# Kernel optimization log

Measured on AMD Instinct MI355X. Metric: run time of the kernel, lower is better.

## Reference

```python
import jax, jax.numpy as jnp
import numpy as np

NUM_CAPSULE = 10
DIM_CAPSULE = 16
ROUTINGS = 3
EPS = 1e-7  # K.epsilon()


def squash(x, axis=-1):
    sq_norm = jnp.sum(jnp.square(x), axis=axis, keepdims=True) + EPS
    coeff = jnp.sqrt(sq_norm) / (1.0 + sq_norm)
    return coeff * x


def setup_inputs() -> dict:
    key = jax.random.key(0)
    k1, k2 = jax.random.split(key)
    B, I, Din = 64, 4096, 128
    u_vecs = jax.random.normal(k1, (B, I, Din), dtype=jnp.float32)
    # glorot-ish scale for the capsule kernel (flattened conv1d kernel of size 1)
    W = jax.random.normal(k2, (Din, NUM_CAPSULE * DIM_CAPSULE), dtype=jnp.float32) * 0.06
    return {"u_vecs": u_vecs, "W": W}


def reference(u_vecs, W):
    B, I, Din = u_vecs.shape
    N, D = NUM_CAPSULE, DIM_CAPSULE
    # conv1d with kernel size 1 == per-position matmul
    u_hat = jnp.einsum('bid,dk->bik', u_vecs, W)          # [B, I, N*D]
    u_hat = u_hat.reshape(B, I, N, D).transpose(0, 2, 1, 3)  # [B, N, I, D]

    b = jnp.zeros((B, N, I), dtype=u_hat.dtype)
    outputs = None
    for i in range(ROUTINGS):
        c = jax.nn.softmax(b, axis=1)                      # softmax over num_capsule
        s = jnp.einsum('bni,bnid->bnd', c, u_hat)          # weighted sum over input caps
        outputs = squash(s)                                # [B, N, D]
        if i < ROUTINGS - 1:
            b = jnp.einsum('bnd,bnid->bni', outputs, u_hat)  # agreement logits
    return outputs
```

## Files before the change

### kernel.cpp

```cpp
#include <hip/hip_runtime.h>
#include <hip/hip_bf16.h>
#include <math.h>

#define NCAP 10
#define DCAP 16
#define DIN  128
#define NPOS 4096
#define NB   64

typedef short short8 __attribute__((ext_vector_type(8)));
typedef float floatx4 __attribute__((ext_vector_type(4)));

__device__ inline float bflo(unsigned v) { return __uint_as_float(v << 16); }
__device__ inline float bfhi(unsigned v) { return __uint_as_float(v & 0xFFFF0000u); }
__device__ inline unsigned short f2bf(float f) {
    unsigned u = __float_as_uint(f);
    return (unsigned short)((u + 0x7FFFu + ((u >> 16) & 1u)) >> 16);
}


__global__ __launch_bounds__(256) void wprep(const float* __restrict__ W,
                                             uint4* __restrict__ WTg) {
    const int cid = blockIdx.x * 256 + threadIdx.x;
    if (cid >= 2560) return;
    const int row = cid >> 4;
    const int csn = cid & 15;
    const int kc = csn ^ (row & 15);
    unsigned p[4];
    #pragma unroll
    for (int e = 0; e < 4; ++e) {
        const float a = W[(kc * 8 + e * 2) * 160 + row];
        const float b = W[(kc * 8 + e * 2 + 1) * 160 + row];
        p[e] = (unsigned)f2bf(a) | ((unsigned)f2bf(b) << 16);
    }
    WTg[cid] = make_uint4(p[0], p[1], p[2], p[3]);
}

__global__ __launch_bounds__(256) void gemm_uhat(const float* __restrict__ u,
                                                 const uint4* __restrict__ WTg,
                                                 uint2* __restrict__ uf2,
                                                 float* __restrict__ partial) {
    const int b = blockIdx.x;
    const int blk = blockIdx.y;
    const int t = threadIdx.x;
    const int l = t & 63;
    const int wv = __builtin_amdgcn_readfirstlane(t >> 6);

    __shared__ uint4 WT4[2560];

    #pragma unroll
    for (int i = 0; i < 10; ++i)
        WT4[t + i * 256] = WTg[t + i * 256];
    __syncthreads();

    float cs[4][8];
    #pragma unroll
    for (int kk = 0; kk < 4; ++kk)
        #pragma unroll
        for (int e = 0; e < 8; ++e) cs[kk][e] = 0.f;

    const short8* wt8 = (const short8*)WT4;
    const float4* u4g = (const float4*)u;

    #pragma unroll 1
    for (int mt = 0; mt < 4; ++mt) {
        const size_t row = (size_t)b * NPOS + blk * 256 + mt * 64 + wv * 16 + (l & 15);
        short8 bfr[4];
        #pragma unroll
        for (int kk = 0; kk < 4; ++kk) {
            const float4 x0 = u4g[row * 32 + kk * 8 + (l >> 4) * 2];
            const float4 x1 = u4g[row * 32 + kk * 8 + (l >> 4) * 2 + 1];
            cs[kk][0] += x0.x; cs[kk][1] += x0.y; cs[kk][2] += x0.z; cs[kk][3] += x0.w;
            cs[kk][4] += x1.x; cs[kk][5] += x1.y; cs[kk][6] += x1.z; cs[kk][7] += x1.w;
            short8 a;
            a[0] = (short)f2bf(x0.x); a[1] = (short)f2bf(x0.y);
            a[2] = (short)f2bf(x0.z); a[3] = (short)f2bf(x0.w);
            a[4] = (short)f2bf(x1.x); a[5] = (short)f2bf(x1.y);
            a[6] = (short)f2bf(x1.z); a[7] = (short)f2bf(x1.w);
            bfr[kk] = a;
        }

        const size_t cell = (((size_t)(b * 16 + blk) * 4 + mt) * 4 + wv) * 10;
        #pragma unroll 2
        for (int n = 0; n < 10; ++n) {
            floatx4 a = {0.f, 0.f, 0.f, 0.f};
            #pragma unroll
            for (int kk = 0; kk < 4; ++kk) {
                const short8 wf = wt8[(n * 16 + (l & 15)) * 16 +
                                      ((kk * 4 + (l >> 4)) ^ (l & 15))];
                a = __builtin_amdgcn_mfma_f32_16x16x32_bf16(wf, bfr[kk], a, 0, 0, 0);
            }
            uint2 pk;
            pk.x = (unsigned)f2bf(a[0]) | ((unsigned)f2bf(a[1]) << 16);
            pk.y = (unsigned)f2bf(a[2]) | ((unsigned)f2bf(a[3]) << 16);
            uf2[(cell + n) * 64 + l] = pk;
        }
    }

    __syncthreads();
    float* csbuf = (float*)WT4;
    #pragma unroll
    for (int kk = 0; kk < 4; ++kk)
        #pragma unroll
        for (int e = 0; e < 8; ++e) {
            float v = cs[kk][e];
            v += __shfl_xor(v, 1); v += __shfl_xor(v, 2);
            v += __shfl_xor(v, 4); v += __shfl_xor(v, 8);
            cs[kk][e] = v;
        }
    if ((l & 15) == 0) {
        #pragma unroll
        for (int kk = 0; kk < 4; ++kk)
            #pragma unroll
            for (int e = 0; e < 8; ++e)
                csbuf[wv * 128 + kk * 32 + (l >> 4) * 8 + e] = cs[kk][e];
    }
    __syncthreads();
    if (t < 128)
        partial[(size_t)(b * 16 + blk) * 128 + t] =
            csbuf[t] + csbuf[128 + t] + csbuf[256 + t] + csbuf[384 + t];
}

__global__ __launch_bounds__(128) void small0(const float* __restrict__ partial,
                                              const float* __restrict__ W,
                                              float* __restrict__ vbuf) {
    const int b = blockIdx.x / NCAP;
    const int n = blockIdx.x % NCAP;
    const int t = threadIdx.x;
    __shared__ float xv[DIN];
    float a = 0.f;
    #pragma unroll 4
    for (int c = 0; c < 16; ++c)
        a += partial[(size_t)(b * 16 + c) * DIN + t];
    xv[t] = a;
    __syncthreads();
    if (t < DCAP) {
        float sv = 0.f;
        for (int d = 0; d < DIN; ++d)
            sv = fmaf(xv[d], W[d * 160 + n * DCAP + t], sv);
        sv *= 0.1f;
        float nq = sv * sv;
        #pragma unroll
        for (int mm = 8; mm >= 1; mm >>= 1) nq += __shfl_xor(nq, mm, 16);
        nq += 1e-7f;
        vbuf[(size_t)(b * NCAP + n) * DCAP + t] = sv * sqrtf(nq) / (1.0f + nq);
    }
}

__global__ __launch_bounds__(256) void route_uf(const uint2* __restrict__ uf2,
                                                const float* __restrict__ vbuf,
                                                float* __restrict__ pws) {
    const int b = blockIdx.x;
    const int g = blockIdx.y;
    const int t = threadIdx.x;
    const int l = t & 63;
    const int w = __builtin_amdgcn_readfirstlane(t >> 6);

    const size_t cell = (((size_t)(b * 16 + (g >> 2)) * 4 + (g & 3)) * 4 + w) * 10;

    float vals[10][4];
    float lg[10];
    #pragma unroll
    for (int n = 0; n < 10; ++n) {
        const uint2 q = uf2[(cell + n) * 64 + l];
        vals[n][0] = bflo(q.x); vals[n][1] = bfhi(q.x);
        vals[n][2] = bflo(q.y); vals[n][3] = bfhi(q.y);
        const float4 vq = *(const float4*)&vbuf[(size_t)(b * 10 + n) * 16 + (l >> 4) * 4];
        lg[n] = vals[n][0] * vq.x + vals[n][1] * vq.y +
                vals[n][2] * vq.z + vals[n][3] * vq.w;
    }
    #pragma unroll
    for (int n = 0; n < 10; ++n) {
        lg[n] += __shfl_xor(lg[n], 16);
        lg[n] += __shfl_xor(lg[n], 32);
    }
    float m = lg[0];
    #pragma unroll
    for (int n = 1; n < 10; ++n) m = fmaxf(m, lg[n]);
    float ssum = 0.f;
    float c[10];
    #pragma unroll
    for (int n = 0; n < 10; ++n) { c[n] = __expf(lg[n] - m); ssum += c[n]; }
    const float inv = 1.0f / ssum;

    float sp[10][4];
    #pragma unroll
    for (int n = 0; n < 10; ++n) {
        const float cn = c[n] * inv;
        #pragma unroll
        for (int r = 0; r < 4; ++r) sp[n][r] = cn * vals[n][r];
    }
    #pragma unroll
    for (int n = 0; n < 10; ++n)
        #pragma unroll
        for (int r = 0; r < 4; ++r) {
            float v = sp[n][r];
            v += __shfl_xor(v, 1); v += __shfl_xor(v, 2);
            v += __shfl_xor(v, 4); v += __shfl_xor(v, 8);
            sp[n][r] = v;
        }

    __shared__ float sm[4][160];
    if ((l & 15) == 0) {
        #pragma unroll
        for (int n = 0; n < 10; ++n)
            #pragma unroll
            for (int r = 0; r < 4; ++r)
                sm[w][n * 16 + (l >> 4) * 4 + r] = sp[n][r];
    }
    __syncthreads();
    if (t < 160)
        pws[(size_t)(b * 64 + g) * 160 + t] =
            sm[0][t] + sm[1][t] + sm[2][t] + sm[3][t];
}

__global__ __launch_bounds__(256) void smallv(const float* __restrict__ pws,
                                              float* __restrict__ dst) {
    const int b = blockIdx.x;
    const int t = threadIdx.x;
    if (t >= 160) return;
    float a = 0.f;
    #pragma unroll 8
    for (int c = 0; c < 64; ++c)
        a += pws[(size_t)(b * 64 + c) * 160 + t];
    float nq = a * a;
    #pragma unroll
    for (int mm = 8; mm >= 1; mm >>= 1) nq += __shfl_xor(nq, mm, 16);
    nq += 1e-7f;
    dst[(size_t)b * 160 + t] = a * sqrtf(nq) / (1.0f + nq);
}


__global__ __launch_bounds__(256) void caps_sum(const float* __restrict__ u,
                                                float* __restrict__ partial) {
    const int b = blockIdx.x;
    const int chunk = blockIdx.y;
    const int t = threadIdx.x;
    const int v4 = t & 31;
    const int prow = t >> 5;
    const float4* up = (const float4*)u;
    const size_t posbase = (size_t)b * NPOS + chunk * 256;
    float4 acc = make_float4(0.f, 0.f, 0.f, 0.f);
    #pragma unroll 8
    for (int j = 0; j < 32; ++j) {
        float4 x = up[(posbase + prow + j * 8) * 32 + v4];
        acc.x += x.x; acc.y += x.y; acc.z += x.z; acc.w += x.w;
    }
    __shared__ float4 red[8][32];
    red[prow][v4] = acc;
    __syncthreads();
    if (t < 32) {
        float4 s = red[0][t];
        #pragma unroll
        for (int r = 1; r < 8; ++r) {
            s.x += red[r][t].x; s.y += red[r][t].y;
            s.z += red[r][t].z; s.w += red[r][t].w;
        }
        ((float4*)partial)[((size_t)b * 16 + chunk) * 32 + t] = s;
    }
}

template <int MODE>
__global__ __launch_bounds__(128) void caps_small(const float* __restrict__ src,
                                                  const float* __restrict__ W,
                                                  float* __restrict__ dst) {
    const int b = blockIdx.x / NCAP;
    const int n = blockIdx.x % NCAP;
    const int t = threadIdx.x;
    __shared__ float xv[DIN];
    __shared__ float vv[DCAP];
    float a = 0.f;
    if (MODE == 0) {
        #pragma unroll 4
        for (int c = 0; c < 16; ++c) a += src[(size_t)(b * 16 + c) * DIN + t];
    } else {
        #pragma unroll 4
        for (int c = 0; c < 16; ++c) a += src[((size_t)(b * 16 + c) * NCAP + n) * DIN + t];
    }
    xv[t] = a;
    __syncthreads();
    if (t < DCAP) {
        float sv = 0.f;
        for (int d = 0; d < DIN; ++d) sv = fmaf(xv[d], W[d * 160 + n * DCAP + t], sv);
        if (MODE == 0) sv *= 0.1f;
        float nq = sv * sv;
        #pragma unroll
        for (int mm = 8; mm >= 1; mm >>= 1) nq += __shfl_xor(nq, mm, 16);
        nq += 1e-7f;
        const float v = sv * sqrtf(nq) / (1.0f + nq);
        if (MODE == 2) dst[(size_t)(b * NCAP + n) * DCAP + t] = v;
        else vv[t] = v;
    }
    if (MODE != 2) {
        __syncthreads();
        float wd = 0.f;
        #pragma unroll
        for (int dd = 0; dd < DCAP; ++dd)
            wd = fmaf(W[t * 160 + n * DCAP + dd], vv[dd], wd);
        dst[(size_t)(b * NCAP + n) * DIN + t] = wd;
    }
}

__global__ __launch_bounds__(256, 3) void caps_route(const float* __restrict__ u,
                                                     const float* __restrict__ wsrc,
                                                     float* __restrict__ pdst) {
    const int b = blockIdx.x;
    const int tile = blockIdx.y;
    const int t = threadIdx.x;
    const int lane = t & 63;
    const int wv = __builtin_amdgcn_readfirstlane(t >> 6);
    __shared__ float4 tl4[64 * 32];
    __shared__ float lgp[4][64][11];
    float* tlf = (float*)tl4;
    const float4* wq4 = (const float4*)(wsrc + (size_t)b * (NCAP * DIN));
    float acc0[NCAP], acc1[NCAP];
    #pragma unroll
    for (int n = 0; n < NCAP; ++n) { acc0[n] = 0.f; acc1[n] = 0.f; }
    for (int s = 0; s < 4; ++s) {
        __syncthreads();
        const float4* src4 = (const float4*)u + ((size_t)b * NPOS + tile * 256 + s * 64) * 32;
        #pragma unroll
        for (int i = 0; i < 8; ++i) {
            const int q = t + i * 256;
            const int r = q >> 5, c = q & 31;
            tl4[r * 32 + (c ^ (r & 7))] = src4[q];
        }
        __syncthreads();
        float lg[NCAP];
        #pragma unroll
        for (int n = 0; n < NCAP; ++n) lg[n] = 0.f;
        #pragma unroll
        for (int j = 0; j < 8; ++j) {
            const float4 u4 = tl4[lane * 32 + wv * 8 + (j ^ (lane & 7))];
            #pragma unroll
            for (int n = 0; n < NCAP; ++n) {
                const float4 w4 = wq4[n * 32 + wv * 8 + j];
                lg[n] = fmaf(u4.x, w4.x, fmaf(u4.y, w4.y,
                        fmaf(u4.z, w4.z, fmaf(u4.w, w4.w, lg[n]))));
            }
        }
        #pragma unroll
        for (int n = 0; n < NCAP; ++n) lgp[wv][lane][n] = lg[n];
        __syncthreads();
        float c[NCAP];
        float m = -1e30f;
        #pragma unroll
        for (int n = 0; n < NCAP; ++n) {
            c[n] = lgp[0][lane][n] + lgp[1][lane][n] + lgp[2][lane][n] + lgp[3][lane][n];
            m = fmaxf(m, c[n]);
        }
        float ssum = 0.f;
        #pragma unroll
        for (int n = 0; n < NCAP; ++n) { c[n] = __expf(c[n] - m); ssum += c[n]; }
        const float inv = 1.0f / ssum;
        #pragma unroll
        for (int n = 0; n < NCAP; ++n) c[n] *= inv;
        const int col0 = lane >> 2, word = lane & 3;
        #pragma unroll
        for (int i = 0; i < 16; ++i) {
            const int p = wv * 16 + i;
            const int ca = col0 ^ (p & 7);
            const float u0 = tlf[(p * 32 + ca) * 4 + word];
            const float u1 = tlf[(p * 32 + ca + 16) * 4 + word];
            #pragma unroll
            for (int n = 0; n < NCAP; ++n) {
                const float cp = __int_as_float(
                    __builtin_amdgcn_readlane(__float_as_int(c[n]), p));
                acc0[n] = fmaf(cp, u0, acc0[n]);
                acc1[n] = fmaf(cp, u1, acc1[n]);
            }
        }
    }
    __syncthreads();
    float* red = tlf;
    #pragma unroll
    for (int n = 0; n < NCAP; ++n) {
        red[(wv * NCAP + n) * DIN + lane]      = acc0[n];
        red[(wv * NCAP + n) * DIN + lane + 64] = acc1[n];
    }
    __syncthreads();
    float* pb = pdst + (size_t)(b * 16 + tile) * (NCAP * DIN);
    for (int k = t; k < NCAP * DIN; k += 256)
        pb[k] = red[k] + red[1280 + k] + red[2560 + k] + red[3840 + k];
}

extern "C" void kernel_launch(void* const* d_in, const int* in_sizes, int n_in,
                              void* d_out, int out_size, void* d_ws, size_t ws_size,
                              hipStream_t stream) {
    const float* u = (const float*)d_in[0];
    const float* W = (const float*)d_in[1];
    float* out = (float*)d_out;
    char* wsb = (char*)d_ws;

    if (ws_size >= 86679552ull) {
        float* partial = (float*)wsb;
        float* pws     = (float*)wsb;
        float* vbuf    = (float*)(wsb + 2621440);
        uint4* WTg     = (uint4*)(wsb + 2662400);
        uint2* uf2     = (uint2*)(wsb + 2703360);

        wprep<<<10, 256, 0, stream>>>(W, WTg);
        gemm_uhat<<<dim3(NB, 16), 256, 0, stream>>>(u, WTg, uf2, partial);
        small0<<<NB * NCAP, 128, 0, stream>>>(partial, W, vbuf);
        route_uf<<<dim3(NB, 64), 256, 0, stream>>>(uf2, vbuf, pws);
        smallv<<<NB, 256, 0, stream>>>(pws, vbuf);
        route_uf<<<dim3(NB, 64), 256, 0, stream>>>(uf2, vbuf, pws);
        smallv<<<NB, 256, 0, stream>>>(pws, out);
    } else {
        float* partial = (float*)wsb;
        float* wbuf    = (float*)wsb + 131072;
        float* pws32   = (float*)wsb + 212992;
        caps_sum<<<dim3(NB, 16), 256, 0, stream>>>(u, partial);
        caps_small<0><<<NB * NCAP, 128, 0, stream>>>(partial, W, wbuf);
        caps_route<<<dim3(NB, 16), 256, 0, stream>>>(u, wbuf, pws32);
        caps_small<1><<<NB * NCAP, 128, 0, stream>>>(pws32, W, wbuf);
        caps_route<<<dim3(NB, 16), 256, 0, stream>>>(u, wbuf, pws32);
        caps_small<2><<<NB * NCAP, 128, 0, stream>>>(pws32, W, out);
    }
}
```

Measured before the change: 133.2 us.

## Drop LDS weight staging in GEMM and restructure routing via shared-memory transpose

The u_hat GEMM stops copying the full bf16 weight matrix into LDS. Each wave now reads its weight fragments straight from global memory (cache) and reuses each fragment across two row tiles, with the grid doubled to 32 blocks per batch and the partial-sum count doubled to match. The routing kernel stages the u_hat tile in LDS, computes logits per wave slice, then reduces across positions with a per-output-column loop instead of cross-lane shuffles. This removes the LDS fill and shuffle reductions but adds LDS traffic, extra barriers and a serial 64-step accumulation done by only 160 threads.

```diff
diff --git a/kernel.cpp b/kernel.cpp
--- a/kernel.cpp
+++ b/kernel.cpp
@@ -17,6 +17,7 @@
     unsigned u = __float_as_uint(f);
     return (unsigned short)((u + 0x7FFFu + ((u >> 16) & 1u)) >> 16);
 }
+__device__ inline float bf2f(unsigned short h) { return __uint_as_float(((unsigned)h) << 16); }
 
 
 __global__ __launch_bounds__(256) void wprep(const float* __restrict__ W,
@@ -46,12 +47,8 @@
     const int l = t & 63;
     const int wv = __builtin_amdgcn_readfirstlane(t >> 6);
 
-    __shared__ uint4 WT4[2560];
-
-    #pragma unroll
-    for (int i = 0; i < 10; ++i)
-        WT4[t + i * 256] = WTg[t + i * 256];
-    __syncthreads();
+    const float4* u4g = (const float4*)u;
+    const short8* wt8g = (const short8*)WTg;
 
     float cs[4][8];
     #pragma unroll
@@ -59,13 +56,10 @@
         #pragma unroll
         for (int e = 0; e < 8; ++e) cs[kk][e] = 0.f;
 
-    const short8* wt8 = (const short8*)WT4;
-    const float4* u4g = (const float4*)u;
-
-    #pragma unroll 1
-    for (int mt = 0; mt < 4; ++mt) {
-        const size_t row = (size_t)b * NPOS + blk * 256 + mt * 64 + wv * 16 + (l & 15);
-        short8 bfr[4];
+    short8 ubf[2][4];
+    #pragma unroll
+    for (int mt = 0; mt < 2; ++mt) {
+        const size_t row = (size_t)b * NPOS + blk * 128 + mt * 64 + wv * 16 + (l & 15);
         #pragma unroll
         for (int kk = 0; kk < 4; ++kk) {
             const float4 x0 = u4g[row * 32 + kk * 8 + (l >> 4) * 2];
@@ -77,28 +71,31 @@
             a[2] = (short)f2bf(x0.z); a[3] = (short)f2bf(x0.w);
             a[4] = (short)f2bf(x1.x); a[5] = (short)f2bf(x1.y);
             a[6] = (short)f2bf(x1.z); a[7] = (short)f2bf(x1.w);
-            bfr[kk] = a;
-        }
-
-        const size_t cell = (((size_t)(b * 16 + blk) * 4 + mt) * 4 + wv) * 10;
-        #pragma unroll 2
-        for (int n = 0; n < 10; ++n) {
+            ubf[mt][kk] = a;
+        }
+    }
+
+    #pragma unroll 2
+    for (int n = 0; n < 10; ++n) {
+        short8 wf[4];
+        #pragma unroll
+        for (int kk = 0; kk < 4; ++kk)
+            wf[kk] = wt8g[(n * 16 + (l & 15)) * 16 + ((kk * 4 + (l >> 4)) ^ (l & 15))];
+        #pragma unroll
+        for (int mt = 0; mt < 2; ++mt) {
             floatx4 a = {0.f, 0.f, 0.f, 0.f};
             #pragma unroll
-            for (int kk = 0; kk < 4; ++kk) {
-                const short8 wf = wt8[(n * 16 + (l & 15)) * 16 +
-                                      ((kk * 4 + (l >> 4)) ^ (l & 15))];
-                a = __builtin_amdgcn_mfma_f32_16x16x32_bf16(wf, bfr[kk], a, 0, 0, 0);
-            }
+            for (int kk = 0; kk < 4; ++kk)
+                a = __builtin_amdgcn_mfma_f32_16x16x32_bf16(wf[kk], ubf[mt][kk], a, 0, 0, 0);
             uint2 pk;
             pk.x = (unsigned)f2bf(a[0]) | ((unsigned)f2bf(a[1]) << 16);
             pk.y = (unsigned)f2bf(a[2]) | ((unsigned)f2bf(a[3]) << 16);
+            const size_t cell = ((size_t)(b * 64 + blk * 2 + mt) * 4 + wv) * 10;
             uf2[(cell + n) * 64 + l] = pk;
         }
     }
 
-    __syncthreads();
-    float* csbuf = (float*)WT4;
+    __shared__ float csbuf[4][128];
     #pragma unroll
     for (int kk = 0; kk < 4; ++kk)
         #pragma unroll
@@ -113,12 +110,12 @@
         for (int kk = 0; kk < 4; ++kk)
             #pragma unroll
             for (int e = 0; e < 8; ++e)
-                csbuf[wv * 128 + kk * 32 + (l >> 4) * 8 + e] = cs[kk][e];
+                csbuf[wv][kk * 32 + (l >> 4) * 8 + e] = cs[kk][e];
     }
     __syncthreads();
     if (t < 128)
-        partial[(size_t)(b * 16 + blk) * 128 + t] =
-            csbuf[t] + csbuf[128 + t] + csbuf[256 + t] + csbuf[384 + t];
+        partial[(size_t)(b * 32 + blk) * 128 + t] =
+            csbuf[0][t] + csbuf[1][t] + csbuf[2][t] + csbuf[3][t];
 }
 
 __global__ __launch_bounds__(128) void small0(const float* __restrict__ partial,
@@ -129,9 +126,9 @@
     const int t = threadIdx.x;
     __shared__ float xv[DIN];
     float a = 0.f;
-    #pragma unroll 4
-    for (int c = 0; c < 16; ++c)
-        a += partial[(size_t)(b * 16 + c) * DIN + t];
+    #pragma unroll 8
+    for (int c = 0; c < 32; ++c)
+        a += partial[(size_t)(b * 32 + c) * DIN + t];
     xv[t] = a;
     __syncthreads();
     if (t < DCAP) {
@@ -156,62 +153,54 @@
     const int l = t & 63;
     const int w = __builtin_amdgcn_readfirstlane(t >> 6);
 
-    const size_t cell = (((size_t)(b * 16 + (g >> 2)) * 4 + (g & 3)) * 4 + w) * 10;
-
-    float vals[10][4];
-    float lg[10];
+    __shared__ __align__(16) short tls[64 * 168];
+    __shared__ float lgp[4][64][10];
+    __shared__ float csm[64][10];
+
+    const size_t base = (size_t)(b * 64 + g) * 2560 + (size_t)w * 640;
+    const int pos = w * 16 + (l & 15);
+    const int d0 = (l >> 4) * 4;
     #pragma unroll
     for (int n = 0; n < 10; ++n) {
-        const uint2 q = uf2[(cell + n) * 64 + l];
-        vals[n][0] = bflo(q.x); vals[n][1] = bfhi(q.x);
-        vals[n][2] = bflo(q.y); vals[n][3] = bfhi(q.y);
-        const float4 vq = *(const float4*)&vbuf[(size_t)(b * 10 + n) * 16 + (l >> 4) * 4];
-        lg[n] = vals[n][0] * vq.x + vals[n][1] * vq.y +
-                vals[n][2] * vq.z + vals[n][3] * vq.w;
-    }
+        const uint2 q = uf2[base + n * 64 + l];
+        *(uint2*)&tls[pos * 168 + n * 16 + d0] = q;
+    }
+    __syncthreads();
+
     #pragma unroll
     for (int n = 0; n < 10; ++n) {
-        lg[n] += __shfl_xor(lg[n], 16);
-        lg[n] += __shfl_xor(lg[n], 32);
-    }
-    float m = lg[0];
-    #pragma unroll
-    for (int n = 1; n < 10; ++n) m = fmaxf(m, lg[n]);
+        const uint2 uu = *(const uint2*)&tls[l * 168 + n * 16 + w * 4];
+        const float4 vq = *(const float4*)&vbuf[(size_t)(b * 10 + n) * 16 + w * 4];
+        lgp[w][l][n] = bflo(uu.x) * vq.x + bfhi(uu.x) * vq.y +
+                       bflo(uu.y) * vq.z + bfhi(uu.y) * vq.w;
+    }
+    __syncthreads();
+
+    float c[10];
+    float m = -1e30f;
+    #pragma unroll
+    for (int n = 0; n < 10; ++n) {
+        c[n] = lgp[0][l][n] + lgp[1][l][n] + lgp[2][l][n] + lgp[3][l][n];
+        m = fmaxf(m, c[n]);
+    }
     float ssum = 0.f;
-    float c[10];
-    #pragma unroll
-    for (int n = 0; n < 10; ++n) { c[n] = __expf(lg[n] - m); ssum += c[n]; }
+    #pragma unroll
+    for (int n = 0; n < 10; ++n) { c[n] = __expf(c[n] - m); ssum += c[n]; }
     const float inv = 1.0f / ssum;
-
-    float sp[10][4];
-    #pragma unroll
-    for (int n = 0; n < 10; ++n) {
-        const float cn = c[n] * inv;
-        #pragma unroll
-        for (int r = 0; r < 4; ++r) sp[n][r] = cn * vals[n][r];
-    }
-    #pragma unroll
-    for (int n = 0; n < 10; ++n)
-        #pragma unroll
-        for (int r = 0; r < 4; ++r) {
-            float v = sp[n][r];
-            v += __shfl_xor(v, 1); v += __shfl_xor(v, 2);
-            v += __shfl_xor(v, 4); v += __shfl_xor(v, 8);
-            sp[n][r] = v;
-        }
-
-    __shared__ float sm[4][160];
-    if ((l & 15) == 0) {
-        #pragma unroll
-        for (int n = 0; n < 10; ++n)
-            #pragma unroll
-            for (int r = 0; r < 4; ++r)
-                sm[w][n * 16 + (l >> 4) * 4 + r] = sp[n][r];
-    }
-    __syncthreads();
-    if (t < 160)
-        pws[(size_t)(b * 64 + g) * 160 + t] =
-            sm[0][t] + sm[1][t] + sm[2][t] + sm[3][t];
+    if (w == 0) {
+        #pragma unroll
+        for (int n = 0; n < 10; ++n) csm[l][n] = c[n] * inv;
+    }
+    __syncthreads();
+
+    if (t < 160) {
+        const int n = t >> 4;
+        float acc = 0.f;
+        #pragma unroll 8
+        for (int p = 0; p < 64; ++p)
+            acc = fmaf(csm[p][n], bf2f((unsigned short)tls[p * 168 + t]), acc);
+        pws[(size_t)(b * 64 + g) * 160 + t] = acc;
+    }
 }
 
 __global__ __launch_bounds__(256) void smallv(const float* __restrict__ pws,
@@ -400,7 +389,7 @@
         uint2* uf2     = (uint2*)(wsb + 2703360);
 
         wprep<<<10, 256, 0, stream>>>(W, WTg);
-        gemm_uhat<<<dim3(NB, 16), 256, 0, stream>>>(u, WTg, uf2, partial);
+        gemm_uhat<<<dim3(NB, 32), 256, 0, stream>>>(u, WTg, uf2, partial);
         small0<<<NB * NCAP, 128, 0, stream>>>(partial, W, vbuf);
         route_uf<<<dim3(NB, 64), 256, 0, stream>>>(uf2, vbuf, pws);
         smallv<<<NB, 256, 0, stream>>>(pws, vbuf);
```

New measurement: 115.5 us. -13.3%, faster.
